# Kernel optimization log

Measured on AMD Instinct MI355X. Metric: run time of the kernel, lower is better.

## Reference

```python
import jax, jax.numpy as jnp
import numpy as np

B, C, H, W, N, NH, DFF = 2, 256, 128, 128, 8, 8, 1024
EPS = 1e-5


def _ln(x, g, b):
    m = jnp.mean(x, -1, keepdims=True)
    v = jnp.mean((x - m) ** 2, -1, keepdims=True)
    return (x - m) / jnp.sqrt(v + EPS) * g + b


def _mha(q, k, v, Wqkv, bqkv, Wo, bo, nh):
    # q,k,v: [Bq, S, C]; torch MultiheadAttention with packed in_proj
    Bq, S, Cd = q.shape
    dh = Cd // nh
    Wq, Wk, Wv = jnp.split(Wqkv, 3, axis=0)
    bq, bk, bv = jnp.split(bqkv, 3, axis=0)
    qp = (q @ Wq.T + bq).reshape(Bq, S, nh, dh).transpose(0, 2, 1, 3)
    kp = (k @ Wk.T + bk).reshape(Bq, S, nh, dh).transpose(0, 2, 1, 3)
    vp = (v @ Wv.T + bv).reshape(Bq, S, nh, dh).transpose(0, 2, 1, 3)
    scores = jnp.einsum('bhqd,bhkd->bhqk', qp, kp) / jnp.sqrt(jnp.asarray(dh, qp.dtype))
    attn = jax.nn.softmax(scores, axis=-1)
    o = jnp.einsum('bhqk,bhkd->bhqd', attn, vp).transpose(0, 2, 1, 3).reshape(Bq, S, Cd)
    return o @ Wo.T + bo


def _enc_layer(q, k, v, Wqkv, bqkv, Wo, bo, W1, b1, W2, b2, g1, be1, g2, be2, nh):
    # normalize_before=False, dropout=0
    src = _ln(v + _mha(q, k, v, Wqkv, bqkv, Wo, bo, nh), g1, be1)
    ffn = jax.nn.relu(src @ W1.T + b1) @ W2.T + b2
    return _ln(src + ffn, g2, be2)


def _encode(feat, pe, layer_params, nh):
    # feat: [Nv, hw, C]; pe = glob_pos + rel_pos broadcast: [Nv, hw, C]
    out = feat
    qk = out + pe
    out = _enc_layer(qk, qk, out, *layer_params, nh)
    out_t = out.transpose(1, 0, 2)                 # [hw, Nv, C] axis-permuted pass
    qk = out_t + pe.transpose(1, 0, 2)
    out = _enc_layer(qk, qk, out_t, *layer_params, nh).transpose(1, 0, 2)
    return out


def _forward(backbone_memory, defe_feature_filtered, glob_pos_embed,
             Wqkv, bqkv, Wo, bo, W1, b1, W2, b2, g1, be1, g2, be2,
             relW1, relb1, relW2, relb2, n):
    Bm, Cd, Hf, Wf = backbone_memory.shape
    h, w = Hf // n, Wf // n
    Nv, hw = n * n, h * w

    # relative position embedding: MLP over normalized grid coords [h,w,2]
    gy, gx = jnp.meshgrid(jnp.arange(h, dtype=jnp.float32),
                          jnp.arange(w, dtype=jnp.float32), indexing='ij')
    coords = jnp.stack([gx / (w - 1), gy / (h - 1)], axis=-1)
    rel = (jax.nn.relu(coords @ relW1.T + relb1) @ relW2.T + relb2)  # [h,w,C]
    rel = rel.reshape(1, hw, Cd)                                      # [1,hw,C]

    # window partition: [B, Nv, hw, C]
    win = backbone_memory.reshape(Bm, Cd, n, h, n, w).transpose(0, 2, 4, 1, 3, 5)
    win = win.reshape(Bm, Nv, Cd, hw).transpose(0, 1, 3, 2)

    # per-window global pos embed: [Nv, hw, C]
    glob = glob_pos_embed.reshape(Cd, n, h, n, w).transpose(1, 3, 0, 2, 4)
    glob = glob.reshape(Nv, Cd, hw).transpose(0, 2, 1)

    pe = glob + rel
    layer_params = (Wqkv, bqkv, Wo, bo, W1, b1, W2, b2, g1, be1, g2, be2)
    enc = jax.vmap(lambda f: _encode(f, pe, layer_params, NH))(win)   # [B,Nv,hw,C]

    # scatter windows back and add residually (reconstructed += feats)
    back = enc.transpose(0, 1, 3, 2).reshape(Bm, n, n, Cd, h, w)
    back = back.transpose(0, 3, 1, 4, 2, 5).reshape(Bm, Cd, Hf, Wf)
    reconstructed = backbone_memory + back

    # defe_mask via non-overlapping max-pool (all-ones mask -> all valid)
    Hm, Wm = defe_feature_filtered.shape[-2:]
    kh = (Hm // Hf) * h
    kw = (Wm // Wf) * w
    pooled = defe_feature_filtered.reshape(Bm, 1, n, kh, n, kw).max(axis=(3, 5))
    defe_mask = pooled[:, 0] > 0
    return reconstructed, defe_mask


def setup_inputs() -> dict:
    key = jax.random.key(0)
    ks = jax.random.split(key, 10)
    s = 0.02
    return {
        'backbone_memory': jax.random.normal(ks[0], (B, C, H, W), jnp.float32),
        'defe_feature_filtered': jnp.ones((B, 1, H, W), jnp.float32),
        'glob_pos_embed': jax.random.normal(ks[1], (C, H, W), jnp.float32),
        'Wqkv': jax.random.normal(ks[2], (3 * C, C), jnp.float32) * s,
        'bqkv': jnp.zeros((3 * C,), jnp.float32),
        'Wo': jax.random.normal(ks[3], (C, C), jnp.float32) * s,
        'bo': jnp.zeros((C,), jnp.float32),
        'W1': jax.random.normal(ks[4], (DFF, C), jnp.float32) * s,
        'b1': jnp.zeros((DFF,), jnp.float32),
        'W2': jax.random.normal(ks[5], (C, DFF), jnp.float32) * s,
        'b2': jnp.zeros((C,), jnp.float32),
        'g1': jnp.ones((C,), jnp.float32),
        'be1': jnp.zeros((C,), jnp.float32),
        'g2': jnp.ones((C,), jnp.float32),
        'be2': jnp.zeros((C,), jnp.float32),
        'relW1': jax.random.normal(ks[6], (64, 2), jnp.float32) * s,
        'relb1': jnp.zeros((64,), jnp.float32),
        'relW2': jax.random.normal(ks[7], (C, 64), jnp.float32) * s,
        'relb2': jnp.zeros((C,), jnp.float32),
        'n': N,
    }


def reference(backbone_memory, defe_feature_filtered, glob_pos_embed,
              Wqkv, bqkv, Wo, bo, W1, b1, W2, b2, g1, be1, g2, be2,
              relW1, relb1, relW2, relb2, n):
    return _forward(backbone_memory, defe_feature_filtered, glob_pos_embed,
                    Wqkv, bqkv, Wo, bo, W1, b1, W2, b2, g1, be1, g2, be2,
                    relW1, relb1, relW2, relb2, n)
```

## Files before the change

### kernel.cpp

```cpp
#include <hip/hip_runtime.h>
#include <hip/hip_bf16.h>

#define C_DIM 256
#define NHEAD 8
#define DH 32
#define NTOK 32768
#define PETOK 16384
#define DFF_DIM 1024
#define LN_EPS 1e-5f

typedef unsigned int u32;
typedef unsigned short ushortT;
using frag_ab = __attribute__((ext_vector_type(8))) short;
using f32x4   = __attribute__((ext_vector_type(4))) float;

__device__ __forceinline__ float bflo(u32 u) { union { u32 i; float f; } c; c.i = u << 16; return c.f; }
__device__ __forceinline__ float bfhi(u32 u) { union { u32 i; float f; } c; c.i = u & 0xffff0000u; return c.f; }
__device__ __forceinline__ float b2f(ushortT u) { union { u32 i; float f; } c; c.i = ((u32)u) << 16; return c.f; }
__device__ __forceinline__ ushortT f2b(float f) {
    __hip_bfloat16 b = __float2bfloat16(f);
    return *reinterpret_cast<ushortT*>(&b);
}
__device__ __forceinline__ u32 packbf(float lo, float hi) {
    return (u32)f2b(lo) | ((u32)f2b(hi) << 16);
}
__device__ __forceinline__ void gload_lds16(const ushortT* g, ushortT* l) {
    __builtin_amdgcn_global_load_lds((const __attribute__((address_space(1))) void*)g,
                                     (__attribute__((address_space(3))) void*)l, 16, 0, 0);
}

__global__ void cvt_all_kernel(const float* __restrict__ Wqkv, const float* __restrict__ Wo,
                               const float* __restrict__ W1, const float* __restrict__ W2,
                               ushortT* __restrict__ dst) {
    const int i = (blockIdx.x * 256 + threadIdx.x) * 4;
    const float* src;
    int off;
    if (i < 196608)      { src = Wqkv; off = 0; }
    else if (i < 262144) { src = Wo;   off = 196608; }
    else if (i < 524288) { src = W1;   off = 262144; }
    else                 { src = W2;   off = 524288; }
    const float4 v = *(const float4*)&src[i - off];
    uint2 o = {packbf(v.x, v.y), packbf(v.z, v.w)};
    *(uint2*)&dst[i] = o;
}

__global__ void rel_kernel(const float* __restrict__ relW1, const float* __restrict__ relb1,
                           const float* __restrict__ relW2, const float* __restrict__ relb2,
                           float* __restrict__ rel) {
    __shared__ float hid[64];
    int t = blockIdx.x;
    int ty = t >> 4, tx = t & 15;
    float cx = tx * (1.0f / 15.0f);
    float cy = ty * (1.0f / 15.0f);
    int c = threadIdx.x;
    if (c < 64) {
        float h = relW1[c * 2 + 0] * cx + relW1[c * 2 + 1] * cy + relb1[c];
        hid[c] = fmaxf(h, 0.0f);
    }
    __syncthreads();
    float acc = relb2[c];
    #pragma unroll
    for (int jj = 0; jj < 64; ++jj) acc = fmaf(hid[jj], relW2[c * 64 + jj], acc);
    rel[t * C_DIM + c] = acc;
}

__global__ __launch_bounds__(256) void pe_kernel(const float* __restrict__ glob,
                                                 const float* __restrict__ rel,
                                                 ushortT* __restrict__ peb) {
    __shared__ float tile[32][129];
    const int y = blockIdx.x;
    const int c0 = blockIdx.y * 32;
    const int i = y >> 4, ty = y & 15;
    const int tid = threadIdx.x;
    const int xl = tid & 127;
    #pragma unroll
    for (int p = 0; p < 16; ++p) {
        const int cl = p * 2 + (tid >> 7);
        tile[cl][xl] = glob[(size_t)(c0 + cl) * 16384 + y * 128 + xl];
    }
    __syncthreads();
    const int cl = tid & 31;
    #pragma unroll
    for (int p = 0; p < 16; ++p) {
        const int x = p * 8 + (tid >> 5);
        const int v = i * 8 + (x >> 4);
        const int t = ty * 16 + (x & 15);
        const float val = tile[cl][x] + rel[t * C_DIM + c0 + cl];
        peb[(size_t)(v * 256 + t) * C_DIM + c0 + cl] = f2b(val);
    }
}

__global__ __launch_bounds__(256) void window_kernel(const float* __restrict__ backbone,
                                                     const ushortT* __restrict__ peb,
                                                     ushortT* __restrict__ Xb,
                                                     ushortT* __restrict__ XPEb) {
    __shared__ float tile[32][129];
    const int y = blockIdx.x;
    const int c0 = blockIdx.y * 32;
    const int b = blockIdx.z;
    const int i = y >> 4, ty = y & 15;
    const int tid = threadIdx.x;
    const int xl = tid & 127;
    #pragma unroll
    for (int p = 0; p < 16; ++p) {
        const int cl = p * 2 + (tid >> 7);
        tile[cl][xl] = backbone[(size_t)b * 4194304 + (size_t)(c0 + cl) * 16384 + y * 128 + xl];
    }
    __syncthreads();
    const int cl = tid & 31;
    #pragma unroll
    for (int p = 0; p < 16; ++p) {
        const int x = p * 8 + (tid >> 5);
        const int v = i * 8 + (x >> 4);
        const int t = ty * 16 + (x & 15);
        const size_t vt = (size_t)(v * 256 + t);
        const size_t tok = (size_t)b * PETOK + vt;
        const float val = tile[cl][x];
        Xb[tok * C_DIM + c0 + cl] = f2b(val);
        XPEb[tok * C_DIM + c0 + cl] = f2b(val + b2f(peb[vt * C_DIM + c0 + cl]));
    }
}

__global__ __launch_bounds__(256) void scatter_kernel(const float* __restrict__ backbone,
                                                      const ushortT* __restrict__ X,
                                                      float* __restrict__ out) {
    __shared__ ushortT tile[128][34];
    const int y = blockIdx.x;
    const int c0 = blockIdx.y * 32;
    const int b = blockIdx.z;
    const int i = y >> 4, ty = y & 15;
    const int tid = threadIdx.x;
    const int cl = tid & 31;
    #pragma unroll
    for (int p = 0; p < 16; ++p) {
        const int x = p * 8 + (tid >> 5);
        const int v = i * 8 + (x >> 4);
        const int t = ty * 16 + (x & 15);
        const size_t tok = (size_t)b * PETOK + v * 256 + t;
        tile[x][cl] = X[tok * C_DIM + c0 + cl];
    }
    __syncthreads();
    const int xl = tid & 127;
    #pragma unroll
    for (int p = 0; p < 16; ++p) {
        const int c = c0 + p * 2 + (tid >> 7);
        const size_t gi = (size_t)b * 4194304 + (size_t)c * 16384 + y * 128 + xl;
        out[gi] = backbone[gi] + b2f(tile[xl][p * 2 + (tid >> 7)]);
    }
}

#define BM 128
#define BN 128
#define BK 32

template<bool QKVMODE, bool RELU>
__global__ __launch_bounds__(256) void gemm_bf16(
        const ushortT* __restrict__ A,
        const ushortT* __restrict__ A2,
        int lda,
        const ushortT* __restrict__ W,
        const float* __restrict__ bias,
        ushortT* __restrict__ Cout, int ldc, int K) {
    __shared__ ushortT As[BM][BK];
    __shared__ ushortT Bs[BN][BK];
    const int nwg = gridDim.x * gridDim.y;
    const int flat = blockIdx.y * gridDim.x + blockIdx.x;
    const int cpx = nwg >> 3;
    const int swz = (flat & 7) * cpx + (flat >> 3);
    const int m0 = (swz / gridDim.x) * BM;
    const int n0 = (swz % gridDim.x) * BN;
    const ushortT* Ause = (QKVMODE && n0 >= 512) ? A2 : A;
    const int tid = threadIdx.x;
    const int lane = tid & 63;
    const int wave = tid >> 6;
    const int wm = (wave >> 1) * 64;
    const int wn = (wave & 1) * 64;
    const int fr = lane & 15;
    const int fg = lane >> 4;
    const int gRow = wave * 32 + (lane >> 2);
    const int gCol = (lane & 3) * 8;

    f32x4 acc[4][4];
    #pragma unroll
    for (int i = 0; i < 4; ++i)
        #pragma unroll
        for (int j = 0; j < 4; ++j)
            acc[i][j] = (f32x4){0.f, 0.f, 0.f, 0.f};

    for (int k0 = 0; k0 < K; k0 += BK) {
        gload_lds16(&Ause[(size_t)(m0 + gRow) * lda + k0 + gCol], &As[wave * 32][0]);
        gload_lds16(&Ause[(size_t)(m0 + gRow + 16) * lda + k0 + gCol], &As[wave * 32 + 16][0]);
        gload_lds16(&W[(size_t)(n0 + gRow) * K + k0 + gCol], &Bs[wave * 32][0]);
        gload_lds16(&W[(size_t)(n0 + gRow + 16) * K + k0 + gCol], &Bs[wave * 32 + 16][0]);
        __syncthreads();
        frag_ab af[4], bf[4];
        #pragma unroll
        for (int i = 0; i < 4; ++i) af[i] = *(const frag_ab*)&As[wm + i * 16 + fr][fg * 8];
        #pragma unroll
        for (int j = 0; j < 4; ++j) bf[j] = *(const frag_ab*)&Bs[wn + j * 16 + fr][fg * 8];
        #pragma unroll
        for (int i = 0; i < 4; ++i)
            #pragma unroll
            for (int j = 0; j < 4; ++j)
                acc[i][j] = __builtin_amdgcn_mfma_f32_16x16x32_bf16(af[i], bf[j], acc[i][j], 0, 0, 0);
        __syncthreads();
    }
    #pragma unroll
    for (int j = 0; j < 4; ++j) {
        const float bv = bias[n0 + wn + j * 16 + fr];
        #pragma unroll
        for (int i = 0; i < 4; ++i) {
            #pragma unroll
            for (int r = 0; r < 4; ++r) {
                float v = acc[i][j][r] + bv;
                if (RELU) v = fmaxf(v, 0.0f);
                const int m = m0 + wm + i * 16 + fg * 4 + r;
                const int n = n0 + wn + j * 16 + fr;
                Cout[(size_t)m * ldc + n] = f2b(v);
            }
        }
    }
}

#define KVC 128
__global__ __launch_bounds__(256) void attn_p0(const ushortT* __restrict__ QKVb,
                                               ushortT* __restrict__ Ob) {
    __shared__ ushortT K_lds[KVC * 40];
    __shared__ ushortT V_t[32 * 136];
    __shared__ ushortT P_lds[4][16 * 136];
    const int grp = blockIdx.x;
    const int h = grp & 7;
    const int bv = grp >> 3;
    const int base = (bv >> 6) * PETOK + (bv & 63) * 256;
    const int tid = threadIdx.x;
    const int wave = tid >> 6;
    const int lane = tid & 63;
    const int fr = lane & 15;
    const int fg = lane >> 4;
    const float scale = 0.17677669529663687f;

    frag_ab qf[4];
    size_t qtok[4];
    #pragma unroll
    for (int s = 0; s < 4; ++s) {
        qtok[s] = (size_t)(base + wave * 64 + s * 16 + fr);
        qf[s] = *(const frag_ab*)&QKVb[qtok[s] * 768 + h * DH + fg * 8];
    }
    float m[4], l[4];
    f32x4 o0[4], o1[4];
    #pragma unroll
    for (int s = 0; s < 4; ++s) {
        m[s] = -1e30f; l[s] = 0.f;
        o0[s] = (f32x4){0.f, 0.f, 0.f, 0.f};
        o1[s] = (f32x4){0.f, 0.f, 0.f, 0.f};
    }

    for (int c = 0; c < 2; ++c) {
        __syncthreads();
        #pragma unroll
        for (int it = 0; it < 2; ++it) {
            const int idx = it * 256 + tid;
            const int row = idx >> 2, ch = idx & 3;
            const size_t tok = (size_t)(base + c * KVC + row);
            const uint4 kv = *(const uint4*)&QKVb[tok * 768 + 256 + h * DH + ch * 8];
            *(uint4*)&K_lds[row * 40 + ch * 8] = kv;
            const uint4 vv = *(const uint4*)&QKVb[tok * 768 + 512 + h * DH + ch * 8];
            const ushortT* vp = (const ushortT*)&vv;
            #pragma unroll
            for (int e = 0; e < 8; ++e) V_t[(ch * 8 + e) * 136 + row] = vp[e];
        }
        __syncthreads();
        #pragma unroll
        for (int s = 0; s < 4; ++s) {
            f32x4 sc[8];
            #pragma unroll
            for (int kt = 0; kt < 8; ++kt) {
                const frag_ab kf = *(const frag_ab*)&K_lds[(kt * 16 + fr) * 40 + fg * 8];
                sc[kt] = __builtin_amdgcn_mfma_f32_16x16x32_bf16(kf, qf[s], (f32x4){0.f, 0.f, 0.f, 0.f}, 0, 0, 0);
            }
            float mx = -1e30f;
            #pragma unroll
            for (int kt = 0; kt < 8; ++kt)
                mx = fmaxf(mx, fmaxf(fmaxf(sc[kt][0], sc[kt][1]), fmaxf(sc[kt][2], sc[kt][3])));
            mx = fmaxf(mx, __shfl_xor(mx, 16, 64));
            mx = fmaxf(mx, __shfl_xor(mx, 32, 64));
            const float nm = fmaxf(m[s], mx);
            const float corr = __expf((m[s] - nm) * scale);
            m[s] = nm;
            float lsum = 0.f;
            #pragma unroll
            for (int kt = 0; kt < 8; ++kt) {
                const float p0 = __expf((sc[kt][0] - nm) * scale);
                const float p1 = __expf((sc[kt][1] - nm) * scale);
                const float p2 = __expf((sc[kt][2] - nm) * scale);
                const float p3 = __expf((sc[kt][3] - nm) * scale);
                lsum += (p0 + p1) + (p2 + p3);
                uint2 pk;
                pk.x = packbf(p0, p1);
                pk.y = packbf(p2, p3);
                *(uint2*)&P_lds[wave][fr * 136 + kt * 16 + fg * 4] = pk;
            }
            lsum += __shfl_xor(lsum, 16, 64);
            lsum += __shfl_xor(lsum, 32, 64);
            l[s] = l[s] * corr + lsum;
            o0[s] *= corr;
            o1[s] *= corr;
            #pragma unroll
            for (int kc = 0; kc < 4; ++kc) {
                const frag_ab pf = *(const frag_ab*)&P_lds[wave][fr * 136 + kc * 32 + fg * 8];
                const frag_ab v0 = *(const frag_ab*)&V_t[fr * 136 + kc * 32 + fg * 8];
                const frag_ab v1 = *(const frag_ab*)&V_t[(16 + fr) * 136 + kc * 32 + fg * 8];
                o0[s] = __builtin_amdgcn_mfma_f32_16x16x32_bf16(v0, pf, o0[s], 0, 0, 0);
                o1[s] = __builtin_amdgcn_mfma_f32_16x16x32_bf16(v1, pf, o1[s], 0, 0, 0);
            }
        }
    }
    #pragma unroll
    for (int s = 0; s < 4; ++s) {
        const float inv = 1.0f / l[s];
        ushortT* ob = &Ob[qtok[s] * C_DIM + h * DH];
        uint2 w0, w1;
        w0.x = packbf(o0[s][0] * inv, o0[s][1] * inv);
        w0.y = packbf(o0[s][2] * inv, o0[s][3] * inv);
        w1.x = packbf(o1[s][0] * inv, o1[s][1] * inv);
        w1.y = packbf(o1[s][2] * inv, o1[s][3] * inv);
        *(uint2*)&ob[fg * 4] = w0;
        *(uint2*)&ob[16 + fg * 4] = w1;
    }
}

__global__ __launch_bounds__(256) void attn_p1(const ushortT* __restrict__ QKVb,
                                               ushortT* __restrict__ Ob) {
    __shared__ ushortT K_lds[4][64 * 40];
    __shared__ ushortT V_t[4][32 * 72];
    __shared__ ushortT P_lds[4][16 * 72];
    const int wave = threadIdx.x >> 6;
    const int lane = threadIdx.x & 63;
    const int unit = blockIdx.x * 4 + wave;
    const int h = unit & 7;
    const int g = unit >> 3;
    const int base = (g >> 8) * PETOK + (g & 255);
    const int fr = lane & 15;
    const int fg = lane >> 4;
    const float scale = 0.17677669529663687f;
    #pragma unroll
    for (int it = 0; it < 4; ++it) {
        const int idx = it * 64 + lane;
        const int row = idx >> 2, ch = idx & 3;
        const size_t tok = (size_t)(base + row * 256);
        const uint4 kv = *(const uint4*)&QKVb[tok * 768 + 256 + h * DH + ch * 8];
        *(uint4*)&K_lds[wave][row * 40 + ch * 8] = kv;
        const uint4 vv = *(const uint4*)&QKVb[tok * 768 + 512 + h * DH + ch * 8];
        const ushortT* vp = (const ushortT*)&vv;
        #pragma unroll
        for (int e = 0; e < 8; ++e) V_t[wave][(ch * 8 + e) * 72 + row] = vp[e];
    }
    #pragma unroll
    for (int s = 0; s < 4; ++s) {
        const int qq = s * 16 + fr;
        const size_t qtok = (size_t)(base + qq * 256);
        const frag_ab qf = *(const frag_ab*)&QKVb[qtok * 768 + h * DH + fg * 8];
        f32x4 sc[4];
        #pragma unroll
        for (int kt = 0; kt < 4; ++kt) {
            const frag_ab kf = *(const frag_ab*)&K_lds[wave][(kt * 16 + fr) * 40 + fg * 8];
            sc[kt] = __builtin_amdgcn_mfma_f32_16x16x32_bf16(kf, qf, (f32x4){0.f, 0.f, 0.f, 0.f}, 0, 0, 0);
        }
        float mx = -1e30f;
        #pragma unroll
        for (int kt = 0; kt < 4; ++kt)
            mx = fmaxf(mx, fmaxf(fmaxf(sc[kt][0], sc[kt][1]), fmaxf(sc[kt][2], sc[kt][3])));
        mx = fmaxf(mx, __shfl_xor(mx, 16, 64));
        mx = fmaxf(mx, __shfl_xor(mx, 32, 64));
        float lsum = 0.f;
        #pragma unroll
        for (int kt = 0; kt < 4; ++kt) {
            const float p0 = __expf((sc[kt][0] - mx) * scale);
            const float p1 = __expf((sc[kt][1] - mx) * scale);
            const float p2 = __expf((sc[kt][2] - mx) * scale);
            const float p3 = __expf((sc[kt][3] - mx) * scale);
            lsum += (p0 + p1) + (p2 + p3);
            uint2 pk;
            pk.x = packbf(p0, p1);
            pk.y = packbf(p2, p3);
            *(uint2*)&P_lds[wave][fr * 72 + kt * 16 + fg * 4] = pk;
        }
        lsum += __shfl_xor(lsum, 16, 64);
        lsum += __shfl_xor(lsum, 32, 64);
        f32x4 o0 = {0.f, 0.f, 0.f, 0.f}, o1 = {0.f, 0.f, 0.f, 0.f};
        #pragma unroll
        for (int kc = 0; kc < 2; ++kc) {
            const frag_ab pf = *(const frag_ab*)&P_lds[wave][fr * 72 + kc * 32 + fg * 8];
            const frag_ab v0 = *(const frag_ab*)&V_t[wave][fr * 72 + kc * 32 + fg * 8];
            const frag_ab v1 = *(const frag_ab*)&V_t[wave][(16 + fr) * 72 + kc * 32 + fg * 8];
            o0 = __builtin_amdgcn_mfma_f32_16x16x32_bf16(v0, pf, o0, 0, 0, 0);
            o1 = __builtin_amdgcn_mfma_f32_16x16x32_bf16(v1, pf, o1, 0, 0, 0);
        }
        const float inv = 1.0f / lsum;
        ushortT* ob = &Ob[qtok * C_DIM + h * DH];
        uint2 w0, w1;
        w0.x = packbf(o0[0] * inv, o0[1] * inv);
        w0.y = packbf(o0[2] * inv, o0[3] * inv);
        w1.x = packbf(o1[0] * inv, o1[1] * inv);
        w1.y = packbf(o1[2] * inv, o1[3] * inv);
        *(uint2*)&ob[fg * 4] = w0;
        *(uint2*)&ob[16 + fg * 4] = w1;
    }
}

template<bool WXPE>
__global__ __launch_bounds__(256) void ln_kernel(ushortT* __restrict__ X, const ushortT* __restrict__ Y,
                                                 const float* __restrict__ g, const float* __restrict__ be,
                                                 const ushortT* __restrict__ peb,
                                                 ushortT* __restrict__ XPE) {
    int tok = blockIdx.x * 4 + (threadIdx.x >> 6);
    int lane = threadIdx.x & 63;
    const uint2 xu = *(const uint2*)&X[(size_t)tok * C_DIM + lane * 4];
    const uint2 yu = *(const uint2*)&Y[(size_t)tok * C_DIM + lane * 4];
    float v0 = bflo(xu.x) + bflo(yu.x), v1 = bfhi(xu.x) + bfhi(yu.x);
    float v2 = bflo(xu.y) + bflo(yu.y), v3 = bfhi(xu.y) + bfhi(yu.y);
    float s = v0 + v1 + v2 + v3;
    float ss = v0 * v0 + v1 * v1 + v2 * v2 + v3 * v3;
    #pragma unroll
    for (int off = 32; off; off >>= 1) {
        s += __shfl_xor(s, off, 64);
        ss += __shfl_xor(ss, off, 64);
    }
    float mean = s * (1.0f / 256.0f);
    float var = ss * (1.0f / 256.0f) - mean * mean;
    float inv = rsqrtf(var + LN_EPS);
    const float4 gv = *(const float4*)&g[lane * 4];
    const float4 bv = *(const float4*)&be[lane * 4];
    float o0 = (v0 - mean) * inv * gv.x + bv.x;
    float o1 = (v1 - mean) * inv * gv.y + bv.y;
    float o2 = (v2 - mean) * inv * gv.z + bv.z;
    float o3 = (v3 - mean) * inv * gv.w + bv.w;
    uint2 ob = {packbf(o0, o1), packbf(o2, o3)};
    *(uint2*)&X[(size_t)tok * C_DIM + lane * 4] = ob;
    if (WXPE) {
        const size_t vt = (size_t)(tok & 16383);
        const uint2 pu = *(const uint2*)&peb[vt * C_DIM + lane * 4];
        uint2 xp;
        xp.x = packbf(o0 + bflo(pu.x), o1 + bfhi(pu.x));
        xp.y = packbf(o2 + bflo(pu.y), o3 + bfhi(pu.y));
        *(uint2*)&XPE[(size_t)tok * C_DIM + lane * 4] = xp;
    }
}

__global__ void mask_kernel(const float* __restrict__ defe, float* __restrict__ out) {
    __shared__ float wmax[4];
    const int idx = blockIdx.x;
    const int b = idx >> 6;
    const int ii = (idx >> 3) & 7;
    const int jj = idx & 7;
    const int t = threadIdx.x;
    const int y = t >> 4, xx = t & 15;
    float v = defe[b * 16384 + (ii * 16 + y) * 128 + jj * 16 + xx];
    #pragma unroll
    for (int off = 32; off; off >>= 1) v = fmaxf(v, __shfl_xor(v, off, 64));
    if ((t & 63) == 0) wmax[t >> 6] = v;
    __syncthreads();
    if (t == 0) {
        float mx = fmaxf(fmaxf(wmax[0], wmax[1]), fmaxf(wmax[2], wmax[3]));
        out[8388608 + idx] = (mx > 0.0f) ? 1.0f : 0.0f;
    }
}

extern "C" void kernel_launch(void* const* d_in, const int* in_sizes, int n_in,
                              void* d_out, int out_size, void* d_ws, size_t ws_size,
                              hipStream_t stream) {
    const float* backbone = (const float*)d_in[0];
    const float* defe     = (const float*)d_in[1];
    const float* glob     = (const float*)d_in[2];
    const float* Wqkv     = (const float*)d_in[3];
    const float* bqkv     = (const float*)d_in[4];
    const float* Wo       = (const float*)d_in[5];
    const float* bo       = (const float*)d_in[6];
    const float* W1       = (const float*)d_in[7];
    const float* b1       = (const float*)d_in[8];
    const float* W2       = (const float*)d_in[9];
    const float* b2       = (const float*)d_in[10];
    const float* g1       = (const float*)d_in[11];
    const float* be1      = (const float*)d_in[12];
    const float* g2       = (const float*)d_in[13];
    const float* be2      = (const float*)d_in[14];
    const float* relW1    = (const float*)d_in[15];
    const float* relb1    = (const float*)d_in[16];
    const float* relW2    = (const float*)d_in[17];
    const float* relb2    = (const float*)d_in[18];

    ushortT* peb    = (ushortT*)d_ws;
    ushortT* Wqkv_b = peb + 4194304;
    ushortT* Wo_b   = Wqkv_b + 196608;
    ushortT* W1_b   = Wo_b + 65536;
    ushortT* W2_b   = W1_b + 262144;
    ushortT* Xb     = W2_b + 262144;
    ushortT* XPEb   = Xb + 8388608;
    ushortT* QKVb   = XPEb + 8388608;
    ushortT* Ob     = QKVb + 25165824;
    ushortT* Hb     = QKVb;
    ushortT* Yb     = Ob + 8388608;
    float*   relf   = (float*)(Yb + 8388608);
    size_t needed = (size_t)((char*)(relf + 65536) - (char*)d_ws);
    if (ws_size < needed) return;

    cvt_all_kernel<<<768, 256, 0, stream>>>(Wqkv, Wo, W1, W2, Wqkv_b);
    rel_kernel<<<256, 256, 0, stream>>>(relW1, relb1, relW2, relb2, relf);
    pe_kernel<<<dim3(128, 8), 256, 0, stream>>>(glob, relf, peb);
    window_kernel<<<dim3(128, 8, 2), 256, 0, stream>>>(backbone, peb, Xb, XPEb);

    for (int pass = 0; pass < 2; ++pass) {
        gemm_bf16<true, false><<<dim3(768 / BN, NTOK / BM), 256, 0, stream>>>(
            XPEb, Xb, C_DIM, Wqkv_b, bqkv, QKVb, 768, C_DIM);
        if (pass == 0) {
            attn_p0<<<128 * NHEAD, 256, 0, stream>>>(QKVb, Ob);
        } else {
            attn_p1<<<4096 / 4, 256, 0, stream>>>(QKVb, Ob);
        }
        gemm_bf16<false, false><<<dim3(256 / BN, NTOK / BM), 256, 0, stream>>>(
            Ob, nullptr, C_DIM, Wo_b, bo, Yb, C_DIM, C_DIM);
        ln_kernel<false><<<NTOK / 4, 256, 0, stream>>>(Xb, Yb, g1, be1, nullptr, nullptr);
        gemm_bf16<false, true><<<dim3(DFF_DIM / BN, NTOK / BM), 256, 0, stream>>>(
            Xb, nullptr, C_DIM, W1_b, b1, Hb, DFF_DIM, C_DIM);
        gemm_bf16<false, false><<<dim3(256 / BN, NTOK / BM), 256, 0, stream>>>(
            Hb, nullptr, DFF_DIM, W2_b, b2, Yb, C_DIM, DFF_DIM);
        if (pass == 0) {
            ln_kernel<true><<<NTOK / 4, 256, 0, stream>>>(Xb, Yb, g2, be2, peb, XPEb);
        } else {
            ln_kernel<false><<<NTOK / 4, 256, 0, stream>>>(Xb, Yb, g2, be2, nullptr, nullptr);
        }
    }

    scatter_kernel<<<dim3(128, 8, 2), 256, 0, stream>>>(backbone, Xb, (float*)d_out);
    mask_kernel<<<128, 256, 0, stream>>>(defe, (float*)d_out);
}
```

Measured before the change: 335.8 us.

## Fuse rel-pos MLP into PE kernel, pack bf16 stores, prefetch KV in attention

Removes the separate rel_kernel launch by computing the relative-position MLP for the needed 16x32 slice inside pe_kernel. It also switches bf16 packing to the paired conversion intrinsic and uses packed conversion in the GEMM epilogue. The pass-0 attention now loads the second KV chunk into registers while the first chunk is computed. The fused MLP is recomputed redundantly across blocks and the prefetch raises register pressure.

After: 350.1 us. 1.04x slower.

```diff
diff --git a/kernel.cpp b/kernel.cpp
--- a/kernel.cpp
+++ b/kernel.cpp
@@ -22,7 +22,9 @@
     return *reinterpret_cast<ushortT*>(&b);
 }
 __device__ __forceinline__ u32 packbf(float lo, float hi) {
-    return (u32)f2b(lo) | ((u32)f2b(hi) << 16);
+    float2 f2 = {lo, hi};
+    __hip_bfloat162 h = __float22bfloat162_rn(f2);
+    return *reinterpret_cast<u32*>(&h);
 }
 __device__ __forceinline__ void gload_lds16(const ushortT* g, ushortT* l) {
     __builtin_amdgcn_global_load_lds((const __attribute__((address_space(1))) void*)g,
@@ -44,30 +46,14 @@
     *(uint2*)&dst[i] = o;
 }
 
-__global__ void rel_kernel(const float* __restrict__ relW1, const float* __restrict__ relb1,
-                           const float* __restrict__ relW2, const float* __restrict__ relb2,
-                           float* __restrict__ rel) {
-    __shared__ float hid[64];
-    int t = blockIdx.x;
-    int ty = t >> 4, tx = t & 15;
-    float cx = tx * (1.0f / 15.0f);
-    float cy = ty * (1.0f / 15.0f);
-    int c = threadIdx.x;
-    if (c < 64) {
-        float h = relW1[c * 2 + 0] * cx + relW1[c * 2 + 1] * cy + relb1[c];
-        hid[c] = fmaxf(h, 0.0f);
-    }
-    __syncthreads();
-    float acc = relb2[c];
-    #pragma unroll
-    for (int jj = 0; jj < 64; ++jj) acc = fmaf(hid[jj], relW2[c * 64 + jj], acc);
-    rel[t * C_DIM + c] = acc;
-}
-
 __global__ __launch_bounds__(256) void pe_kernel(const float* __restrict__ glob,
-                                                 const float* __restrict__ rel,
+                                                 const float* __restrict__ relW1,
+                                                 const float* __restrict__ relb1,
+                                                 const float* __restrict__ relW2,
+                                                 const float* __restrict__ relb2,
                                                  ushortT* __restrict__ peb) {
     __shared__ float tile[32][129];
+    __shared__ float relv[16][33];
     const int y = blockIdx.x;
     const int c0 = blockIdx.y * 32;
     const int i = y >> 4, ty = y & 15;
@@ -78,6 +64,21 @@
         const int cl = p * 2 + (tid >> 7);
         tile[cl][xl] = glob[(size_t)(c0 + cl) * 16384 + y * 128 + xl];
     }
+    const float cy = ty * (1.0f / 15.0f);
+    #pragma unroll
+    for (int p = 0; p < 2; ++p) {
+        const int idx = p * 256 + tid;
+        const int tl = idx >> 5;
+        const int cl = idx & 31;
+        const float cx = tl * (1.0f / 15.0f);
+        float acc = relb2[c0 + cl];
+        #pragma unroll 8
+        for (int j = 0; j < 64; ++j) {
+            const float hh = fmaxf(relW1[j * 2] * cx + relW1[j * 2 + 1] * cy + relb1[j], 0.0f);
+            acc = fmaf(hh, relW2[(c0 + cl) * 64 + j], acc);
+        }
+        relv[tl][cl] = acc;
+    }
     __syncthreads();
     const int cl = tid & 31;
     #pragma unroll
@@ -85,7 +86,7 @@
         const int x = p * 8 + (tid >> 5);
         const int v = i * 8 + (x >> 4);
         const int t = ty * 16 + (x & 15);
-        const float val = tile[cl][x] + rel[t * C_DIM + c0 + cl];
+        const float val = tile[cl][x] + relv[x & 15][cl];
         peb[(size_t)(v * 256 + t) * C_DIM + c0 + cl] = f2b(val);
     }
 }
@@ -207,16 +208,19 @@
     }
     #pragma unroll
     for (int j = 0; j < 4; ++j) {
-        const float bv = bias[n0 + wn + j * 16 + fr];
+        const int n = n0 + wn + j * 16 + fr;
+        const float bv = bias[n];
         #pragma unroll
         for (int i = 0; i < 4; ++i) {
-            #pragma unroll
-            for (int r = 0; r < 4; ++r) {
-                float v = acc[i][j][r] + bv;
-                if (RELU) v = fmaxf(v, 0.0f);
-                const int m = m0 + wm + i * 16 + fg * 4 + r;
-                const int n = n0 + wn + j * 16 + fr;
-                Cout[(size_t)m * ldc + n] = f2b(v);
+            const int mb = m0 + wm + i * 16 + fg * 4;
+            #pragma unroll
+            for (int r2 = 0; r2 < 2; ++r2) {
+                float a0 = acc[i][j][2 * r2] + bv;
+                float a1 = acc[i][j][2 * r2 + 1] + bv;
+                if (RELU) { a0 = fmaxf(a0, 0.0f); a1 = fmaxf(a1, 0.0f); }
+                const u32 u = packbf(a0, a1);
+                Cout[(size_t)(mb + 2 * r2) * ldc + n] = (ushortT)u;
+                Cout[(size_t)(mb + 2 * r2 + 1) * ldc + n] = (ushortT)(u >> 16);
             }
         }
     }
@@ -255,21 +259,28 @@
         o1[s] = (f32x4){0.f, 0.f, 0.f, 0.f};
     }
 
-    for (int c = 0; c < 2; ++c) {
-        __syncthreads();
+    auto loadc = [&](int c, uint4* kk, uint4* vv) {
         #pragma unroll
         for (int it = 0; it < 2; ++it) {
             const int idx = it * 256 + tid;
             const int row = idx >> 2, ch = idx & 3;
             const size_t tok = (size_t)(base + c * KVC + row);
-            const uint4 kv = *(const uint4*)&QKVb[tok * 768 + 256 + h * DH + ch * 8];
-            *(uint4*)&K_lds[row * 40 + ch * 8] = kv;
-            const uint4 vv = *(const uint4*)&QKVb[tok * 768 + 512 + h * DH + ch * 8];
-            const ushortT* vp = (const ushortT*)&vv;
+            kk[it] = *(const uint4*)&QKVb[tok * 768 + 256 + h * DH + ch * 8];
+            vv[it] = *(const uint4*)&QKVb[tok * 768 + 512 + h * DH + ch * 8];
+        }
+    };
+    auto stage = [&](const uint4* kk, const uint4* vv) {
+        #pragma unroll
+        for (int it = 0; it < 2; ++it) {
+            const int idx = it * 256 + tid;
+            const int row = idx >> 2, ch = idx & 3;
+            *(uint4*)&K_lds[row * 40 + ch * 8] = kk[it];
+            const ushortT* vp = (const ushortT*)&vv[it];
             #pragma unroll
             for (int e = 0; e < 8; ++e) V_t[(ch * 8 + e) * 136 + row] = vp[e];
         }
-        __syncthreads();
+    };
+    auto compute_chunk = [&]() {
         #pragma unroll
         for (int s = 0; s < 4; ++s) {
             f32x4 sc[8];
@@ -314,7 +325,19 @@
                 o1[s] = __builtin_amdgcn_mfma_f32_16x16x32_bf16(v1, pf, o1[s], 0, 0, 0);
             }
         }
-    }
+    };
+
+    uint4 k0r[2], v0r[2], k1r[2], v1r[2];
+    loadc(0, k0r, v0r);
+    stage(k0r, v0r);
+    __syncthreads();
+    loadc(1, k1r, v1r);
+    compute_chunk();
+    __syncthreads();
+    stage(k1r, v1r);
+    __syncthreads();
+    compute_chunk();
+
     #pragma unroll
     for (int s = 0; s < 4; ++s) {
         const float inv = 1.0f / l[s];
@@ -500,13 +523,11 @@
     ushortT* Ob     = QKVb + 25165824;
     ushortT* Hb     = QKVb;
     ushortT* Yb     = Ob + 8388608;
-    float*   relf   = (float*)(Yb + 8388608);
-    size_t needed = (size_t)((char*)(relf + 65536) - (char*)d_ws);
+    size_t needed = (size_t)((char*)(Yb + 8388608) - (char*)d_ws);
     if (ws_size < needed) return;
 
     cvt_all_kernel<<<768, 256, 0, stream>>>(Wqkv, Wo, W1, W2, Wqkv_b);
-    rel_kernel<<<256, 256, 0, stream>>>(relW1, relb1, relW2, relb2, relf);
-    pe_kernel<<<dim3(128, 8), 256, 0, stream>>>(glob, relf, peb);
+    pe_kernel<<<dim3(128, 8), 256, 0, stream>>>(glob, relW1, relb1, relW2, relb2, peb);
     window_kernel<<<dim3(128, 8, 2), 256, 0, stream>>>(backbone, peb, Xb, XPEb);
 
     for (int pass = 0; pass < 2; ++pass) {
```
